# Kernel optimization log

Measured on AMD Instinct MI355X. Metric: run time of the kernel, lower is better.

The kernel has to match this reference:

```python
import jax, jax.numpy as jnp
import numpy as np

# --- config (mirrors the torch/keras module's config object) ---
RATIOS = np.array([0.5, 1.0, 2.0], dtype=np.float32)
SCALE = 128.0
POS_THRESH = 0.15
NMS_THRESH = 0.7
STRIDE = 16.0
H = W = 64
A = len(RATIOS)           # anchors per spatial location
N = H * W * A             # total anchors = 12288


def _conv(x, w, b):
    # NHWC input, HWIO kernel, SAME padding, stride 1
    y = jax.lax.conv_general_dilated(x, w, (1, 1), 'SAME',
                                     dimension_numbers=('NHWC', 'HWIO', 'NHWC'))
    return y + b


def _grid_anchors():
    ws = SCALE * np.sqrt(RATIOS)
    hs = SCALE / np.sqrt(RATIOS)
    base = np.stack([-ws / 2, -hs / 2, ws / 2, hs / 2], axis=1)      # [A,4]
    xs = (np.arange(W, dtype=np.float32) + 0.5) * STRIDE
    ys = (np.arange(H, dtype=np.float32) + 0.5) * STRIDE
    cx, cy = np.meshgrid(xs, ys)                                     # [H,W]
    shifts = np.stack([cx, cy, cx, cy], axis=-1).reshape(-1, 1, 4)   # [H*W,1,4]
    return jnp.asarray((shifts + base[None]).reshape(-1, 4).astype(np.float32))  # [N,4]


def _decode(anchors, deltas):
    # standard RPN box decode: (dx,dy,dw,dh) applied to (x1,y1,x2,y2) anchors
    w = anchors[:, 2] - anchors[:, 0]
    h = anchors[:, 3] - anchors[:, 1]
    xc = (anchors[:, 0] + anchors[:, 2]) * 0.5 + deltas[:, 0] * w
    yc = (anchors[:, 1] + anchors[:, 3]) * 0.5 + deltas[:, 1] * h
    nw = w * jnp.exp(deltas[:, 2])
    nh = h * jnp.exp(deltas[:, 3])
    return jnp.stack([xc - nw / 2, yc - nh / 2, xc + nw / 2, yc + nh / 2], axis=1)  # [N,4]


def _nms(boxes, keep0, thresh):
    # greedy NMS in index order (original passes scores=ones to tf NMS, so
    # the sort by score is a no-op and greedy order == index order).
    boxes = jax.lax.stop_gradient(boxes)
    x1, y1, x2, y2 = boxes[:, 0], boxes[:, 1], boxes[:, 2], boxes[:, 3]
    areas = (x2 - x1) * (y2 - y1)
    idx = jnp.arange(boxes.shape[0])

    def body(i, keep):
        xx1 = jnp.maximum(x1[i], x1)
        yy1 = jnp.maximum(y1[i], y1)
        xx2 = jnp.minimum(x2[i], x2)
        yy2 = jnp.minimum(y2[i], y2)
        inter = jnp.maximum(xx2 - xx1, 0.0) * jnp.maximum(yy2 - yy1, 0.0)
        iou = inter / (areas[i] + areas - inter + 1e-9)
        suppress = keep[i] & keep & (iou > thresh) & (idx > i)
        return keep & ~suppress

    return jax.lax.fori_loop(0, boxes.shape[0], body, keep0)


def setup_inputs() -> dict:
    key = jax.random.key(0)
    ks = jax.random.split(key, 7)
    c_in, c_mid = 1024, 512
    inputs = jax.random.normal(ks[0], (1, H, W, c_in), dtype=jnp.float32)
    conv_w = jax.random.normal(ks[1], (3, 3, c_in, c_mid), dtype=jnp.float32) * 0.01
    conv_b = jnp.zeros((c_mid,), dtype=jnp.float32)
    cls_w = jax.random.normal(ks[2], (1, 1, c_mid, 2 * A), dtype=jnp.float32) * 0.05
    cls_b = jnp.zeros((2 * A,), dtype=jnp.float32)
    reg_w = jax.random.normal(ks[3], (1, 1, c_mid, 4 * A), dtype=jnp.float32) * 0.01
    reg_b = jnp.zeros((4 * A,), dtype=jnp.float32)
    return {"inputs": inputs, "conv_w": conv_w, "conv_b": conv_b,
            "cls_w": cls_w, "cls_b": cls_b, "reg_w": reg_w, "reg_b": reg_b}


def reference(inputs, conv_w, conv_b, cls_w, cls_b, reg_w, reg_b):
    x = jax.nn.relu(_conv(inputs, conv_w, conv_b))                  # [1,H,W,512]
    cls = jax.nn.softmax(_conv(x, cls_w, cls_b), axis=-1)           # [1,H,W,2A]
    reg = _conv(x, reg_w, reg_b)                                    # [1,H,W,4A]
    scores = cls.reshape(-1, 2)[:, 1]                               # [N] fg prob
    deltas = reg.reshape(-1, 4)                                     # [N,4]
    boxes = _decode(_grid_anchors(), deltas)                        # [N,4]
    keep0 = scores > POS_THRESH
    keep = _nms(boxes, keep0, NMS_THRESH)                           # [N] bool
    # fixed-shape proposal output: suppressed / filtered boxes zeroed out
    return boxes * keep[:, None].astype(boxes.dtype)
```

## Files before the change

### kernel.cpp

```cpp
#include <hip/hip_runtime.h>
#include <cstdint>

#define NBOX 12288
#define NWORDS 192
#define POS_THRESH 0.15f
#define NMS_THRESH 0.7f

typedef unsigned long long u64;
typedef _Float16 half8 __attribute__((ext_vector_type(8)));
typedef float floatx4 __attribute__((ext_vector_type(4)));

__global__ __launch_bounds__(256) void zero_y(float4* __restrict__ Y) {
  Y[blockIdx.x * 256 + threadIdx.x] = float4{0.f, 0.f, 0.f, 0.f};
}

__global__ __launch_bounds__(256) void prep_wt(
    const float* __restrict__ Wc, _Float16* __restrict__ WTh, _Float16* __restrict__ WTl)
{
  __shared__ float tile[64][65];
  const int b = blockIdx.x;
  const int tap = b >> 7;
  const int rem = b & 127;
  const int c0 = (rem >> 3) * 64, n0 = (rem & 7) * 64;
  const int t = threadIdx.x;
  #pragma unroll
  for (int i = 0; i < 16; ++i) {
    const int idx = i * 256 + t;
    const int c = idx >> 6, n = idx & 63;
    tile[n][c] = Wc[((size_t)(tap * 1024 + c0 + c)) * 512 + n0 + n];
  }
  __syncthreads();
  #pragma unroll
  for (int i = 0; i < 16; ++i) {
    const int idx = i * 256 + t;
    const int n = idx >> 6, c = idx & 63;
    const float v = tile[n][c];
    const _Float16 h = (_Float16)v;
    const _Float16 l = (_Float16)((v - (float)h) * 4096.0f);
    const size_t o = ((size_t)(tap * 512 + n0 + n)) * 1024 + c0 + c;
    WTh[o] = h;
    WTl[o] = l;
  }
}

#define AROW 40
#define AS_PLANE (4 * 66 * AROW)
#define BS_PLANE (128 * AROW)
#define YPLANE 2097152
__global__ __launch_bounds__(256, 2) void conv_mfma(
    const float* __restrict__ X, const _Float16* __restrict__ WTh,
    const _Float16* __restrict__ WTl, float* __restrict__ Y, int partial)
{
  __shared__ _Float16 As[2 * AS_PLANE];
  __shared__ _Float16 Bs[2 * BS_PLANE];
  const int bid = blockIdx.x;
  const int ks = bid & 3;
  const int nt = (bid >> 2) & 3;
  const int mt = bid >> 4;
  const int t = threadIdx.x;
  const int lane = t & 63, wid = t >> 6;
  const int wm = wid >> 1, wn = wid & 1;
  const int lrow = lane & 15, quad = lane >> 4;

  floatx4 accH[4][4], accL[4][4];
  #pragma unroll
  for (int i = 0; i < 4; ++i)
    #pragma unroll
    for (int j = 0; j < 4; ++j) { accH[i][j] = (floatx4)0.f; accL[i][j] = (floatx4)0.f; }

  for (int kc = 0; kc < 8; ++kc) {
    const int c0 = ks * 256 + kc * 32;
    __syncthreads();
    for (int r = t; r < 264; r += 256) {
      const int yy = r / 66;
      const int xx = r - yy * 66;
      const int yi = mt * 2 + yy - 1;
      const int xi = xx - 1;
      const int akey = (r >> 3) & 3;
      _Float16* dsth = &As[r * AROW];
      _Float16* dstl = dsth + AS_PLANE;
      if (yi >= 0 && yi < 64 && xi >= 0 && xi < 64) {
        const float4* src = (const float4*)(X + ((size_t)(yi * 64 + xi)) * 1024 + c0);
        #pragma unroll
        for (int j = 0; j < 4; ++j) {
          const float4 va = src[2 * j], vb = src[2 * j + 1];
          const float f[8] = {va.x, va.y, va.z, va.w, vb.x, vb.y, vb.z, vb.w};
          half8 hh, hl;
          #pragma unroll
          for (int e = 0; e < 8; ++e) {
            const _Float16 h = (_Float16)f[e];
            hh[e] = h;
            hl[e] = (_Float16)((f[e] - (float)h) * 4096.0f);
          }
          const int sl = (j ^ akey) * 8;
          *(half8*)&dsth[sl] = hh;
          *(half8*)&dstl[sl] = hl;
        }
      } else {
        const half8 z = (half8)(_Float16)0.f;
        #pragma unroll
        for (int j = 0; j < 4; ++j) { *(half8*)&dsth[j * 8] = z; *(half8*)&dstl[j * 8] = z; }
      }
    }
    for (int tap = 0; tap < 9; ++tap) {
      if (tap > 0) __syncthreads();
      {
        const int hl = t >> 7, n = t & 127;
        const int bkey = (n >> 3) & 3;
        const _Float16* src = (hl ? WTl : WTh) +
            ((size_t)(tap * 512 + nt * 128 + n)) * 1024 + c0;
        _Float16* dst = &Bs[hl * BS_PLANE + n * AROW];
        #pragma unroll
        for (int j = 0; j < 4; ++j)
          *(half8*)&dst[(j ^ bkey) * 8] = *(const half8*)&src[j * 8];
      }
      __syncthreads();
      const int dy = tap / 3 - 1, dx = tap - (tap / 3) * 3 - 1;
      const int yy = wm + dy + 1;
      const int xxb = dx + 1;
      half8 Ah[4], Al[4], Bh[4], Bl[4];
      #pragma unroll
      for (int fm = 0; fm < 4; ++fm) {
        const int row = yy * 66 + xxb + fm * 16 + lrow;
        const int idx = row * AROW + ((quad ^ ((row >> 3) & 3)) * 8);
        Ah[fm] = *(const half8*)&As[idx];
        Al[fm] = *(const half8*)&As[idx + AS_PLANE];
      }
      #pragma unroll
      for (int fn = 0; fn < 4; ++fn) {
        const int row = wn * 64 + fn * 16 + lrow;
        const int idx = row * AROW + ((quad ^ ((row >> 3) & 3)) * 8);
        Bh[fn] = *(const half8*)&Bs[idx];
        Bl[fn] = *(const half8*)&Bs[idx + BS_PLANE];
      }
      #pragma unroll
      for (int fm = 0; fm < 4; ++fm)
        #pragma unroll
        for (int fn = 0; fn < 4; ++fn) {
          accH[fm][fn] = __builtin_amdgcn_mfma_f32_16x16x32_f16(Ah[fm], Bh[fn], accH[fm][fn], 0, 0, 0);
          accL[fm][fn] = __builtin_amdgcn_mfma_f32_16x16x32_f16(Al[fm], Bh[fn], accL[fm][fn], 0, 0, 0);
          accL[fm][fn] = __builtin_amdgcn_mfma_f32_16x16x32_f16(Ah[fm], Bl[fn], accL[fm][fn], 0, 0, 0);
        }
    }
  }
  const int m0 = mt * 128 + wm * 64;
  const int n0 = nt * 128 + wn * 64;
  if (partial) {
    float* Yp = Y + (size_t)ks * YPLANE;
    #pragma unroll
    for (int fm = 0; fm < 4; ++fm)
      #pragma unroll
      for (int fn = 0; fn < 4; ++fn) {
        const int n = n0 + fn * 16 + lrow;
        #pragma unroll
        for (int r = 0; r < 4; ++r) {
          const int m = m0 + fm * 16 + quad * 4 + r;
          Yp[(size_t)m * 512 + n] = accH[fm][fn][r] + accL[fm][fn][r] * (1.0f / 4096.0f);
        }
      }
  } else {
    #pragma unroll
    for (int fm = 0; fm < 4; ++fm)
      #pragma unroll
      for (int fn = 0; fn < 4; ++fn) {
        const int n = n0 + fn * 16 + lrow;
        #pragma unroll
        for (int r = 0; r < 4; ++r) {
          const int m = m0 + fm * 16 + quad * 4 + r;
          atomicAdd(&Y[(size_t)m * 512 + n],
                    accH[fm][fn][r] + accL[fm][fn][r] * (1.0f / 4096.0f));
        }
      }
  }
}

__global__ __launch_bounds__(64) void heads_decode(
    const float* __restrict__ Yx, int nparts, const float* __restrict__ Bc,
    const float* __restrict__ Wcls, const float* __restrict__ bcls,
    const float* __restrict__ Wreg, const float* __restrict__ breg,
    float* __restrict__ boxes, float* __restrict__ scores, int* __restrict__ ext)
{
  __shared__ float xs[512];
  const int pos = blockIdx.x;
  const int l = threadIdx.x;
  if (l == 0 && pos < NWORDS) ext[pos] = pos;
  float4 v0 = {0.f, 0.f, 0.f, 0.f};
  float4 v1 = {0.f, 0.f, 0.f, 0.f};
  for (int p = 0; p < nparts; ++p) {
    const float* xrow = Yx + (size_t)p * YPLANE + (size_t)pos * 512;
    const float4 a = *(const float4*)&xrow[l * 8];
    const float4 b = *(const float4*)&xrow[l * 8 + 4];
    v0.x += a.x; v0.y += a.y; v0.z += a.z; v0.w += a.w;
    v1.x += b.x; v1.y += b.y; v1.z += b.z; v1.w += b.w;
  }
  const float4 b0 = *(const float4*)&Bc[l * 8];
  const float4 b1 = *(const float4*)&Bc[l * 8 + 4];
  xs[l * 8 + 0] = fmaxf(v0.x + b0.x, 0.f);
  xs[l * 8 + 1] = fmaxf(v0.y + b0.y, 0.f);
  xs[l * 8 + 2] = fmaxf(v0.z + b0.z, 0.f);
  xs[l * 8 + 3] = fmaxf(v0.w + b0.w, 0.f);
  xs[l * 8 + 4] = fmaxf(v1.x + b1.x, 0.f);
  xs[l * 8 + 5] = fmaxf(v1.y + b1.y, 0.f);
  xs[l * 8 + 6] = fmaxf(v1.z + b1.z, 0.f);
  xs[l * 8 + 7] = fmaxf(v1.w + b1.w, 0.f);
  __syncthreads();

  const float* wp;
  int oc;
  float bini;
  if (l < 6)       { wp = Wcls + l;       oc = 6;  bini = bcls[l]; }
  else if (l < 18) { wp = Wreg + (l - 6); oc = 12; bini = breg[l - 6]; }
  else             { wp = Wcls;           oc = 0;  bini = 0.f; }
  float acc = bini;
  const float* p = wp;
  #pragma unroll 4
  for (int c = 0; c < 512; ++c) { acc = fmaf(xs[c], *p, acc); p += oc; }

  const float l0 = __shfl(acc, 0), l1 = __shfl(acc, 1), l2 = __shfl(acc, 2);
  const float l3 = __shfl(acc, 3), l4 = __shfl(acc, 4), l5 = __shfl(acc, 5);
  const int a = (l < 3) ? l : 0;
  const float d0 = __shfl(acc, 6 + a * 4 + 0);
  const float d1 = __shfl(acc, 6 + a * 4 + 1);
  const float d2 = __shfl(acc, 6 + a * 4 + 2);
  const float d3 = __shfl(acc, 6 + a * 4 + 3);

  const float mx = fmaxf(fmaxf(fmaxf(l0, l1), fmaxf(l2, l3)), fmaxf(l4, l5));
  const float e0 = expf(l0 - mx), e1 = expf(l1 - mx), e2 = expf(l2 - mx);
  const float e3 = expf(l3 - mx), e4 = expf(l4 - mx), e5 = expf(l5 - mx);
  const float den = ((((e0 + e1) + e2) + e3) + e4) + e5;
  const float esel = (a == 0) ? e1 : ((a == 1) ? e3 : e5);
  const float sc = esel / den;

  const int px = pos & 63, py = pos >> 6;
  const float cx = (px + 0.5f) * 16.0f;
  const float cy = (py + 0.5f) * 16.0f;
  const float ratio = (a == 0) ? 0.5f : ((a == 1) ? 1.0f : 2.0f);
  const float sq = sqrtf(ratio);
  const float wsz = 128.0f * sq;
  const float hsz = 128.0f / sq;
  const float a0 = cx - wsz * 0.5f;
  const float a1 = cy - hsz * 0.5f;
  const float a2 = cx + wsz * 0.5f;
  const float a3 = cy + hsz * 0.5f;
  const float w = a2 - a0, h = a3 - a1;
  const float xc = __fadd_rn(__fmul_rn(__fadd_rn(a0, a2), 0.5f), __fmul_rn(d0, w));
  const float yc = __fadd_rn(__fmul_rn(__fadd_rn(a1, a3), 0.5f), __fmul_rn(d1, h));
  const float nw = __fmul_rn(w, expf(d2));
  const float nh = __fmul_rn(h, expf(d3));
  float4 box;
  box.x = __fsub_rn(xc, __fmul_rn(nw, 0.5f));
  box.y = __fsub_rn(yc, __fmul_rn(nh, 0.5f));
  box.z = __fadd_rn(xc, __fmul_rn(nw, 0.5f));
  box.w = __fadd_rn(yc, __fmul_rn(nh, 0.5f));

  if (l < 3) {
    const int idx = pos * 3 + a;
    *(float4*)&boxes[idx * 4] = box;
    scores[idx] = sc;
  }
}

__global__ __launch_bounds__(256) void build_mask(
    const float* __restrict__ boxes, u64* __restrict__ maskT,
    int* __restrict__ ext)
{
  const int w  = blockIdx.x;
  const int ci = blockIdx.y;
  if (w < ci) return;
  __shared__ float4 rb[64];
  __shared__ int anyf;
  const int t = threadIdx.x;
  const int lane = t & 63, wid = t >> 6;
  if (t == 0) anyf = 0;
  if (t < 64) rb[t] = *(const float4*)&boxes[(ci * 64 + t) * 4];
  const float4 cb = *(const float4*)&boxes[(w * 64 + lane) * 4];
  const float careaa = __fmul_rn(cb.z - cb.x, cb.w - cb.y);
  const int jglob = w * 64 + lane;
  __syncthreads();
  bool any = false;
  for (int rr = 0; rr < 16; ++rr) {
    const int r = wid * 16 + rr;
    const int row = ci * 64 + r;
    const float4 rx = rb[r];
    const float ra = __fmul_rn(rx.z - rx.x, rx.w - rx.y);
    const float xx1 = fmaxf(rx.x, cb.x);
    const float yy1 = fmaxf(rx.y, cb.y);
    const float xx2 = fminf(rx.z, cb.z);
    const float yy2 = fminf(rx.w, cb.w);
    const float iw = fmaxf(__fsub_rn(xx2, xx1), 0.f);
    const float ih = fmaxf(__fsub_rn(yy2, yy1), 0.f);
    const float inter = __fmul_rn(iw, ih);
    const float den = __fadd_rn(__fsub_rn(__fadd_rn(ra, careaa), inter), 1e-9f);
    const float iou = __fdiv_rn(inter, den);
    const bool bit = (iou > NMS_THRESH) && (jglob > row);
    any |= bit;
    const u64 word = __ballot(bit ? 1 : 0);
    if (lane == 0) maskT[(size_t)w * NBOX + row] = word;
  }
  if (any) anyf = 1;
  __syncthreads();
  if (t == 0 && anyf && w > ci) atomicMax(&ext[ci], w);
}

__device__ __forceinline__ u64 rl64(unsigned lo, unsigned hi, int l) {
  const unsigned a = (unsigned)__builtin_amdgcn_readlane((int)lo, l);
  const unsigned b = (unsigned)__builtin_amdgcn_readlane((int)hi, l);
  return ((u64)b << 32) | (u64)a;
}

#define NSTEP(C_, MU, DU, MP, DP)                                               \
  do {                                                                          \
    const int c_ = (C_);                                                        \
    const int e_ = extS[c_];                                                    \
    const u64 aw0v_ = alive[c_];                                                \
           \
    if (c_ + 1 < NWORDS) {                                                      \
      DP = maskT[(size_t)(c_ + 1) * NBOX + (size_t)(c_ + 1) * 64 + lane];       \
      const int en_ = extS[c_ + 1];                                             \
      const int t0n_ = c_ + 2 + wsub;                                           \
      if (t0n_ <= en_) {                                                        \
        const u64* cbp_ = maskT + (size_t)t0n_ * NBOX + (size_t)(c_ + 1) * 64 + sub * 8; \
        MP##0 = cbp_[0]; MP##1 = cbp_[1]; MP##2 = cbp_[2]; MP##3 = cbp_[3];     \
        MP##4 = cbp_[4]; MP##5 = cbp_[5]; MP##6 = cbp_[6]; MP##7 = cbp_[7];     \
      }                                                                         \
    }                                                                           \
     \
    const unsigned awlo_ = (unsigned)__builtin_amdgcn_readfirstlane((int)(unsigned)(aw0v_ & 0xffffffffull)); \
    const unsigned awhi_ = (unsigned)__builtin_amdgcn_readfirstlane((int)(unsigned)(aw0v_ >> 32)); \
    const u64 aw0_ = ((u64)awhi_ << 32) | (u64)awlo_;                           \
    if (aw0_) {                                                                 \
      const unsigned dlo_ = (unsigned)(DU & 0xffffffffull);                     \
      const unsigned dhi_ = (unsigned)(DU >> 32);                               \
      u64 aw_ = aw0_;                                                           \
      const bool sb_ = ((aw0_ >> lane) & 1ull) && ((DU & aw0_) != 0ull);        \
      u64 pending_ = __ballot(sb_ ? 1 : 0);                                     \
      while (pending_) {                                                        \
        const u64 p0_ = pending_;                                               \
        const u64 p1_ = p0_ & (p0_ - 1);                                        \
        const u64 p2_ = p1_ & (p1_ - 1);                                        \
        const u64 p3_ = p2_ & (p2_ - 1);                                        \
        const int b0_ = __builtin_ctzll(p0_);                                   \
        const int b1_ = p1_ ? __builtin_ctzll(p1_) : 64;                        \
        const int b2_ = p2_ ? __builtin_ctzll(p2_) : 64;                        \
        const int b3_ = p3_ ? __builtin_ctzll(p3_) : 64;                        \
        const u64 r0_ = rl64(dlo_, dhi_, b0_);                                  \
        const u64 r1_ = rl64(dlo_, dhi_, b1_ & 63);                             \
        const u64 r2_ = rl64(dlo_, dhi_, b2_ & 63);                             \
        const u64 r3_ = rl64(dlo_, dhi_, b3_ & 63);                             \
        u64 supp_ = r0_;                                                        \
        u64 done_ = 1ull << b0_;                                                \
        const u64 k1_ = ((b1_ < 64) & !((supp_ >> (b1_ & 63)) & 1ull)) ? ~0ull : 0ull; \
        supp_ |= r1_ & k1_;  done_ |= (1ull << (b1_ & 63)) & k1_;               \
        const u64 k2_ = ((b2_ < 64) & !((supp_ >> (b2_ & 63)) & 1ull)) ? ~0ull : 0ull; \
        supp_ |= r2_ & k2_;  done_ |= (1ull << (b2_ & 63)) & k2_;               \
        const u64 k3_ = ((b3_ < 64) & !((supp_ >> (b3_ & 63)) & 1ull)) ? ~0ull : 0ull; \
        supp_ |= r3_ & k3_;  done_ |= (1ull << (b3_ & 63)) & k3_;               \
        aw_ &= ~supp_;                                                          \
        pending_ &= ~(supp_ | done_);                                           \
      }                                                                         \
       \
      const int t0_ = c_ + 1 + wsub;                                            \
      if (t0_ <= e_) {                                                          \
        const unsigned oct_ = (unsigned)(aw_ >> (sub * 8)) & 0xffu;             \
        u64 sup_ = 0ull;                                                        \
        if (oct_ & 1u)   sup_ |= MU##0;                                         \
        if (oct_ & 2u)   sup_ |= MU##1;                                         \
        if (oct_ & 4u)   sup_ |= MU##2;                                         \
        if (oct_ & 8u)   sup_ |= MU##3;                                         \
        if (oct_ & 16u)  sup_ |= MU##4;                                         \
        if (oct_ & 32u)  sup_ |= MU##5;                                         \
        if (oct_ & 64u)  sup_ |= MU##6;                                         \
        if (oct_ & 128u) sup_ |= MU##7;                                         \
        if (sup_) atomicAnd((unsigned long long*)&alive[t0_], ~sup_);           \
      }                                                                         \
             \
      for (int base_ = c_ + 33; base_ <= e_; base_ += 32) {                     \
        const int tw_ = base_ + wsub;                                           \
        if (tw_ <= e_) {                                                        \
          const u64* cbp_ = maskT + (size_t)tw_ * NBOX + (size_t)c_ * 64 + sub * 8; \
          u64 m_[8];                                                            \
          _Pragma("unroll")                                                     \
          for (int j_ = 0; j_ < 8; ++j_) m_[j_] = cbp_[j_];                     \
          const unsigned oct_ = (unsigned)(aw_ >> (sub * 8)) & 0xffu;           \
          u64 sup_ = 0ull;                                                      \
          _Pragma("unroll")                                                     \
          for (int j_ = 0; j_ < 8; ++j_) if ((oct_ >> j_) & 1u) sup_ |= m_[j_]; \
          if (sup_) atomicAnd((unsigned long long*)&alive[tw_], ~sup_);         \
        }                                                                       \
      }                                                                         \
      if (t == 0) alive[c_] = aw_;                                              \
    }                                                                           \
         \
    asm volatile("s_waitcnt lgkmcnt(0)" ::: "memory");                          \
    __builtin_amdgcn_s_barrier();                                               \
    asm volatile("" ::: "memory");                                              \
  } while (0)

__global__ __launch_bounds__(256) void nms_scan(
    const float* __restrict__ scores, const u64* __restrict__ maskT,
    const int* __restrict__ ext, u64* __restrict__ aliveOut)
{
  __shared__ u64 alive[NWORDS];
  __shared__ int extS[NWORDS];
  const int t = threadIdx.x;
  const int lane = t & 63;
  const int wsub = t >> 3;
  const int sub = t & 7;
  if (t < NWORDS) {
    u64 wbits = 0ull;
    const float4* sp = (const float4*)(scores + t * 64);
    #pragma unroll
    for (int q = 0; q < 16; ++q) {
      const float4 s = sp[q];
      if (s.x > POS_THRESH) wbits |= (1ull << (q * 4 + 0));
      if (s.y > POS_THRESH) wbits |= (1ull << (q * 4 + 1));
      if (s.z > POS_THRESH) wbits |= (1ull << (q * 4 + 2));
      if (s.w > POS_THRESH) wbits |= (1ull << (q * 4 + 3));
    }
    alive[t] = wbits;
    extS[t] = ext[t];
  }
  u64 mA0 = 0, mA1 = 0, mA2 = 0, mA3 = 0, mA4 = 0, mA5 = 0, mA6 = 0, mA7 = 0;
  u64 mB0 = 0, mB1 = 0, mB2 = 0, mB3 = 0, mB4 = 0, mB5 = 0, mB6 = 0, mB7 = 0;
  u64 dgA = 0, dgB = 0;
  const int e0 = ext[0];
  if (1 + wsub <= e0) {
    const u64* cbp = maskT + (size_t)(1 + wsub) * NBOX + sub * 8;
    mA0 = cbp[0]; mA1 = cbp[1]; mA2 = cbp[2]; mA3 = cbp[3];
    mA4 = cbp[4]; mA5 = cbp[5]; mA6 = cbp[6]; mA7 = cbp[7];
  }
  dgA = maskT[lane];
  asm volatile("s_waitcnt lgkmcnt(0)" ::: "memory");
  __builtin_amdgcn_s_barrier();
  asm volatile("" ::: "memory");

  for (int c = 0; c < NWORDS; c += 2) {
    NSTEP(c,     mA, dgA, mB, dgB);
    NSTEP(c + 1, mB, dgB, mA, dgA);
  }
  if (t < NWORDS) aliveOut[t] = alive[t];
}

__global__ __launch_bounds__(256) void write_output(
    const float* __restrict__ boxes, const u64* __restrict__ alive,
    float* __restrict__ out)
{
  const int i = blockIdx.x * 256 + threadIdx.x;
  if (i < NBOX) {
    const bool k = (alive[i >> 6] >> (i & 63)) & 1ull;
    const float4 b = *(const float4*)&boxes[i * 4];
    const float4 z = {0.f, 0.f, 0.f, 0.f};
    *(float4*)&out[i * 4] = k ? b : z;
  }
}

extern "C" void kernel_launch(void* const* d_in, const int* in_sizes, int n_in,
                              void* d_out, int out_size, void* d_ws, size_t ws_size,
                              hipStream_t stream) {
  const float* X    = (const float*)d_in[0];
  const float* Wc   = (const float*)d_in[1];
  const float* Bc   = (const float*)d_in[2];
  const float* Wcls = (const float*)d_in[3];
  const float* bcls = (const float*)d_in[4];
  const float* Wreg = (const float*)d_in[5];
  const float* breg = (const float*)d_in[6];

  char* ws = (char*)d_ws;
  const size_t NEED_BIG = 52676864ull;

  if (ws_size >= NEED_BIG) {
    float*     Y4     = (float*)    (ws);
    float*     boxes  = (float*)    (ws + 33554432);
    float*     scores = (float*)    (ws + 33751040);
    u64*       aliveG = (u64*)      (ws + 33800192);
    int*       extG   = (int*)      (ws + 33801728);
    _Float16*  WTh    = (_Float16*) (ws + 33802496);
    _Float16*  WTl    = (_Float16*) (ws + 43239680);
    u64*       maskT  = (u64*)      (ws + 33802496);

    prep_wt     <<<1152, 256, 0, stream>>>(Wc, WTh, WTl);
    conv_mfma   <<<512, 256, 0, stream>>>(X, WTh, WTl, Y4, 1);
    heads_decode<<<4096, 64, 0, stream>>>(Y4, 4, Bc, Wcls, bcls, Wreg, breg, boxes, scores, extG);
    build_mask  <<<dim3(192, 192), 256, 0, stream>>>(boxes, maskT, extG);
    nms_scan    <<<1, 256, 0, stream>>>(scores, maskT, extG, aliveG);
    write_output<<<48, 256, 0, stream>>>(boxes, aliveG, (float*)d_out);
  } else {
    float*     Y      = (float*)    (ws);
    float*     boxes  = (float*)    (ws + 8388608);
    float*     scores = (float*)    (ws + 8585216);
    u64*       aliveG = (u64*)      (ws + 8634368);
    int*       extG   = (int*)      (ws + 8635904);
    _Float16*  WTh    = (_Float16*) (ws + 8636672);
    _Float16*  WTl    = (_Float16*) (ws + 18073856);
    u64*       maskT  = (u64*)      (ws + 8636672);

    zero_y      <<<2048, 256, 0, stream>>>((float4*)Y);
    prep_wt     <<<1152, 256, 0, stream>>>(Wc, WTh, WTl);
    conv_mfma   <<<512, 256, 0, stream>>>(X, WTh, WTl, Y, 0);
    heads_decode<<<4096, 64, 0, stream>>>(Y, 1, Bc, Wcls, bcls, Wreg, breg, boxes, scores, extG);
    build_mask  <<<dim3(192, 192), 256, 0, stream>>>(boxes, maskT, extG);
    nms_scan    <<<1, 256, 0, stream>>>(scores, maskT, extG, aliveG);
    write_output<<<48, 256, 0, stream>>>(boxes, aliveG, (float*)d_out);
  }
}
```

Before: 501.7 us.

## Replace serial NMS scan with parallel fixed-point iteration and sequential fallback

Result: faster. 490.5 us (-2.2%).

```diff
diff --git a/kernel.cpp b/kernel.cpp
--- a/kernel.cpp
+++ b/kernel.cpp
@@ -307,138 +307,253 @@
   const unsigned b = (unsigned)__builtin_amdgcn_readlane((int)hi, l);
   return ((u64)b << 32) | (u64)a;
 }
-
-#define NSTEP(C_, MU, DU, MP, DP)                                               \
+__device__ __forceinline__ u64 rl64v(u64 v, int ln) {
+  const unsigned a = (unsigned)__builtin_amdgcn_readlane((int)(unsigned)v, ln);
+  const unsigned b = (unsigned)__builtin_amdgcn_readlane((int)(unsigned)(v >> 32), ln);
+  return ((u64)b << 32) | (u64)a;
+}
+__device__ __forceinline__ u64 shflxor64(u64 v, int m) {
+  const int lo = __shfl_xor((int)(unsigned)v, m);
+  const int hi = __shfl_xor((int)(unsigned)(v >> 32), m);
+  return ((u64)(unsigned)hi << 32) | (unsigned)lo;
+}
+__device__ __forceinline__ u64 build_alive(const float* sp) {
+  u64 w = 0ull;
+  const float4* p = (const float4*)sp;
+  #pragma unroll
+  for (int q = 0; q < 16; ++q) {
+    const float4 s = p[q];
+    if (s.x > POS_THRESH) w |= (1ull << (q * 4 + 0));
+    if (s.y > POS_THRESH) w |= (1ull << (q * 4 + 1));
+    if (s.z > POS_THRESH) w |= (1ull << (q * 4 + 2));
+    if (s.w > POS_THRESH) w |= (1ull << (q * 4 + 3));
+  }
+  return w;
+}
+
+#define NSTEPF(C_, MU, DU, MP, DP)                                              \
   do {                                                                          \
-    const int c_ = (C_);                                                        \
-    const int e_ = extS[c_];                                                    \
-    const u64 aw0v_ = alive[c_];                                                \
-           \
-    if (c_ + 1 < NWORDS) {                                                      \
-      DP = maskT[(size_t)(c_ + 1) * NBOX + (size_t)(c_ + 1) * 64 + lane];       \
-      const int en_ = extS[c_ + 1];                                             \
-      const int t0n_ = c_ + 2 + wsub;                                           \
-      if (t0n_ <= en_) {                                                        \
-        const u64* cbp_ = maskT + (size_t)t0n_ * NBOX + (size_t)(c_ + 1) * 64 + sub * 8; \
-        MP##0 = cbp_[0]; MP##1 = cbp_[1]; MP##2 = cbp_[2]; MP##3 = cbp_[3];     \
-        MP##4 = cbp_[4]; MP##5 = cbp_[5]; MP##6 = cbp_[6]; MP##7 = cbp_[7];     \
+    if (t < 256) {                                                              \
+      const int c_ = (C_);                                                      \
+      const int e_ = extS[c_];                                                  \
+      const u64 aw0v_ = alvS[c_];                                               \
+      if (c_ + 1 < NWORDS) {                                                    \
+        DP = maskT[(size_t)(c_ + 1) * NBOX + (size_t)(c_ + 1) * 64 + lane];     \
+        const int en_ = extS[c_ + 1];                                           \
+        const int t0n_ = c_ + 2 + wsub;                                         \
+        if (t0n_ <= en_) {                                                      \
+          const u64* cbp_ = maskT + (size_t)t0n_ * NBOX + (size_t)(c_ + 1) * 64 + sub * 8; \
+          MP##0 = cbp_[0]; MP##1 = cbp_[1]; MP##2 = cbp_[2]; MP##3 = cbp_[3];   \
+          MP##4 = cbp_[4]; MP##5 = cbp_[5]; MP##6 = cbp_[6]; MP##7 = cbp_[7];   \
+        }                                                                       \
+      }                                                                         \
+      const unsigned awlo_ = (unsigned)__builtin_amdgcn_readfirstlane((int)(unsigned)(aw0v_ & 0xffffffffull)); \
+      const unsigned awhi_ = (unsigned)__builtin_amdgcn_readfirstlane((int)(unsigned)(aw0v_ >> 32)); \
+      const u64 aw0_ = ((u64)awhi_ << 32) | (u64)awlo_;                         \
+      if (aw0_) {                                                               \
+        const unsigned dlo_ = (unsigned)(DU & 0xffffffffull);                   \
+        const unsigned dhi_ = (unsigned)(DU >> 32);                             \
+        u64 aw_ = aw0_;                                                         \
+        const bool sb_ = ((aw0_ >> lane) & 1ull) && ((DU & aw0_) != 0ull);      \
+        u64 pending_ = __ballot(sb_ ? 1 : 0);                                   \
+        while (pending_) {                                                      \
+          const u64 p0_ = pending_;                                             \
+          const u64 p1_ = p0_ & (p0_ - 1);                                      \
+          const u64 p2_ = p1_ & (p1_ - 1);                                      \
+          const u64 p3_ = p2_ & (p2_ - 1);                                      \
+          const int b0_ = __builtin_ctzll(p0_);                                 \
+          const int b1_ = p1_ ? __builtin_ctzll(p1_) : 64;                      \
+          const int b2_ = p2_ ? __builtin_ctzll(p2_) : 64;                      \
+          const int b3_ = p3_ ? __builtin_ctzll(p3_) : 64;                      \
+          const u64 r0_ = rl64(dlo_, dhi_, b0_);                                \
+          const u64 r1_ = rl64(dlo_, dhi_, b1_ & 63);                           \
+          const u64 r2_ = rl64(dlo_, dhi_, b2_ & 63);                           \
+          const u64 r3_ = rl64(dlo_, dhi_, b3_ & 63);                           \
+          u64 supp_ = r0_;                                                      \
+          u64 done_ = 1ull << b0_;                                              \
+          const u64 k1_ = ((b1_ < 64) & !((supp_ >> (b1_ & 63)) & 1ull)) ? ~0ull : 0ull; \
+          supp_ |= r1_ & k1_;  done_ |= (1ull << (b1_ & 63)) & k1_;             \
+          const u64 k2_ = ((b2_ < 64) & !((supp_ >> (b2_ & 63)) & 1ull)) ? ~0ull : 0ull; \
+          supp_ |= r2_ & k2_;  done_ |= (1ull << (b2_ & 63)) & k2_;             \
+          const u64 k3_ = ((b3_ < 64) & !((supp_ >> (b3_ & 63)) & 1ull)) ? ~0ull : 0ull; \
+          supp_ |= r3_ & k3_;  done_ |= (1ull << (b3_ & 63)) & k3_;             \
+          aw_ &= ~supp_;                                                        \
+          pending_ &= ~(supp_ | done_);                                         \
+        }                                                                       \
+        const int t0_ = c_ + 1 + wsub;                                          \
+        if (t0_ <= e_) {                                                        \
+          const unsigned oct_ = (unsigned)(aw_ >> (sub * 8)) & 0xffu;           \
+          u64 sup_ = 0ull;                                                      \
+          if (oct_ & 1u)   sup_ |= MU##0;                                       \
+          if (oct_ & 2u)   sup_ |= MU##1;                                       \
+          if (oct_ & 4u)   sup_ |= MU##2;                                       \
+          if (oct_ & 8u)   sup_ |= MU##3;                                       \
+          if (oct_ & 16u)  sup_ |= MU##4;                                       \
+          if (oct_ & 32u)  sup_ |= MU##5;                                       \
+          if (oct_ & 64u)  sup_ |= MU##6;                                       \
+          if (oct_ & 128u) sup_ |= MU##7;                                       \
+          if (sup_) atomicAnd((unsigned long long*)&alvS[t0_], ~sup_);          \
+        }                                                                       \
+        for (int base_ = c_ + 33; base_ <= e_; base_ += 32) {                   \
+          const int tw_ = base_ + wsub;                                         \
+          if (tw_ <= e_) {                                                      \
+            const u64* cbp_ = maskT + (size_t)tw_ * NBOX + (size_t)c_ * 64 + sub * 8; \
+            u64 m_[8];                                                          \
+            _Pragma("unroll")                                                   \
+            for (int j_ = 0; j_ < 8; ++j_) m_[j_] = cbp_[j_];                   \
+            const unsigned oct_ = (unsigned)(aw_ >> (sub * 8)) & 0xffu;         \
+            u64 sup_ = 0ull;                                                    \
+            _Pragma("unroll")                                                   \
+            for (int j_ = 0; j_ < 8; ++j_) if ((oct_ >> j_) & 1u) sup_ |= m_[j_]; \
+            if (sup_) atomicAnd((unsigned long long*)&alvS[tw_], ~sup_);        \
+          }                                                                     \
+        }                                                                       \
+        if (t == 0) alvS[c_] = aw_;                                             \
       }                                                                         \
     }                                                                           \
-     \
-    const unsigned awlo_ = (unsigned)__builtin_amdgcn_readfirstlane((int)(unsigned)(aw0v_ & 0xffffffffull)); \
-    const unsigned awhi_ = (unsigned)__builtin_amdgcn_readfirstlane((int)(unsigned)(aw0v_ >> 32)); \
-    const u64 aw0_ = ((u64)awhi_ << 32) | (u64)awlo_;                           \
-    if (aw0_) {                                                                 \
-      const unsigned dlo_ = (unsigned)(DU & 0xffffffffull);                     \
-      const unsigned dhi_ = (unsigned)(DU >> 32);                               \
-      u64 aw_ = aw0_;                                                           \
-      const bool sb_ = ((aw0_ >> lane) & 1ull) && ((DU & aw0_) != 0ull);        \
-      u64 pending_ = __ballot(sb_ ? 1 : 0);                                     \
-      while (pending_) {                                                        \
-        const u64 p0_ = pending_;                                               \
-        const u64 p1_ = p0_ & (p0_ - 1);                                        \
-        const u64 p2_ = p1_ & (p1_ - 1);                                        \
-        const u64 p3_ = p2_ & (p2_ - 1);                                        \
-        const int b0_ = __builtin_ctzll(p0_);                                   \
-        const int b1_ = p1_ ? __builtin_ctzll(p1_) : 64;                        \
-        const int b2_ = p2_ ? __builtin_ctzll(p2_) : 64;                        \
-        const int b3_ = p3_ ? __builtin_ctzll(p3_) : 64;                        \
-        const u64 r0_ = rl64(dlo_, dhi_, b0_);                                  \
-        const u64 r1_ = rl64(dlo_, dhi_, b1_ & 63);                             \
-        const u64 r2_ = rl64(dlo_, dhi_, b2_ & 63);                             \
-        const u64 r3_ = rl64(dlo_, dhi_, b3_ & 63);                             \
-        u64 supp_ = r0_;                                                        \
-        u64 done_ = 1ull << b0_;                                                \
-        const u64 k1_ = ((b1_ < 64) & !((supp_ >> (b1_ & 63)) & 1ull)) ? ~0ull : 0ull; \
-        supp_ |= r1_ & k1_;  done_ |= (1ull << (b1_ & 63)) & k1_;               \
-        const u64 k2_ = ((b2_ < 64) & !((supp_ >> (b2_ & 63)) & 1ull)) ? ~0ull : 0ull; \
-        supp_ |= r2_ & k2_;  done_ |= (1ull << (b2_ & 63)) & k2_;               \
-        const u64 k3_ = ((b3_ < 64) & !((supp_ >> (b3_ & 63)) & 1ull)) ? ~0ull : 0ull; \
-        supp_ |= r3_ & k3_;  done_ |= (1ull << (b3_ & 63)) & k3_;               \
-        aw_ &= ~supp_;                                                          \
-        pending_ &= ~(supp_ | done_);                                           \
-      }                                                                         \
-       \
-      const int t0_ = c_ + 1 + wsub;                                            \
-      if (t0_ <= e_) {                                                          \
-        const unsigned oct_ = (unsigned)(aw_ >> (sub * 8)) & 0xffu;             \
-        u64 sup_ = 0ull;                                                        \
-        if (oct_ & 1u)   sup_ |= MU##0;                                         \
-        if (oct_ & 2u)   sup_ |= MU##1;                                         \
-        if (oct_ & 4u)   sup_ |= MU##2;                                         \
-        if (oct_ & 8u)   sup_ |= MU##3;                                         \
-        if (oct_ & 16u)  sup_ |= MU##4;                                         \
-        if (oct_ & 32u)  sup_ |= MU##5;                                         \
-        if (oct_ & 64u)  sup_ |= MU##6;                                         \
-        if (oct_ & 128u) sup_ |= MU##7;                                         \
-        if (sup_) atomicAnd((unsigned long long*)&alive[t0_], ~sup_);           \
-      }                                                                         \
-             \
-      for (int base_ = c_ + 33; base_ <= e_; base_ += 32) {                     \
-        const int tw_ = base_ + wsub;                                           \
-        if (tw_ <= e_) {                                                        \
-          const u64* cbp_ = maskT + (size_t)tw_ * NBOX + (size_t)c_ * 64 + sub * 8; \
-          u64 m_[8];                                                            \
-          _Pragma("unroll")                                                     \
-          for (int j_ = 0; j_ < 8; ++j_) m_[j_] = cbp_[j_];                     \
-          const unsigned oct_ = (unsigned)(aw_ >> (sub * 8)) & 0xffu;           \
-          u64 sup_ = 0ull;                                                      \
-          _Pragma("unroll")                                                     \
-          for (int j_ = 0; j_ < 8; ++j_) if ((oct_ >> j_) & 1u) sup_ |= m_[j_]; \
-          if (sup_) atomicAnd((unsigned long long*)&alive[tw_], ~sup_);         \
-        }                                                                       \
-      }                                                                         \
-      if (t == 0) alive[c_] = aw_;                                              \
-    }                                                                           \
-         \
     asm volatile("s_waitcnt lgkmcnt(0)" ::: "memory");                          \
     __builtin_amdgcn_s_barrier();                                               \
     asm volatile("" ::: "memory");                                              \
   } while (0)
 
-__global__ __launch_bounds__(256) void nms_scan(
+__global__ __launch_bounds__(1024) void nms_scan(
     const float* __restrict__ scores, const u64* __restrict__ maskT,
     const int* __restrict__ ext, u64* __restrict__ aliveOut)
 {
-  __shared__ u64 alive[NWORDS];
-  __shared__ int extS[NWORDS];
+  __shared__ u64 alvA[NWORDS], alvB[NWORDS], keep0S[NWORDS];
+  __shared__ int extS[NWORDS], srcLoS[NWORDS];
+  __shared__ int changedS;
   const int t = threadIdx.x;
   const int lane = t & 63;
+  const int wv = t >> 6;
+  const int g = lane >> 3;
+  const int s = lane & 7;
   const int wsub = t >> 3;
   const int sub = t & 7;
+
   if (t < NWORDS) {
-    u64 wbits = 0ull;
-    const float4* sp = (const float4*)(scores + t * 64);
-    #pragma unroll
-    for (int q = 0; q < 16; ++q) {
-      const float4 s = sp[q];
-      if (s.x > POS_THRESH) wbits |= (1ull << (q * 4 + 0));
-      if (s.y > POS_THRESH) wbits |= (1ull << (q * 4 + 1));
-      if (s.z > POS_THRESH) wbits |= (1ull << (q * 4 + 2));
-      if (s.w > POS_THRESH) wbits |= (1ull << (q * 4 + 3));
+    const u64 wb = build_alive(scores + (size_t)t * 64);
+    keep0S[t] = wb;
+    alvA[t] = wb;
+    extS[t] = ext[t];
+  }
+  if (t == 0) changedS = 0;
+  __syncthreads();
+  if (t < NWORDS) {
+    int lo = t;
+    for (int c = 0; c < t; ++c) if (extS[c] >= t) { lo = c; break; }
+    srcLoS[t] = lo;
+  }
+  __syncthreads();
+
+  int cur = 0, converged = 0;
+  for (int it = 0; it < 64; ++it) {
+    const u64* aOld = cur ? alvB : alvA;
+    u64* aNew = cur ? alvA : alvB;
+    for (int k = 0; k < 12; ++k) {
+      const int w = wv + k * 16;
+      const u64 dg = maskT[(size_t)w * NBOX + (size_t)w * 64 + lane];
+      const int lo = srcLoS[w];
+      u64 supx = 0ull;
+      for (int base = lo; base < w; base += 8) {
+        const int c = base + g;
+        u64 part = 0ull;
+        if (c < w) {
+          const u64 av = aOld[c];
+          const unsigned oct = (unsigned)((av >> (s * 8)) & 0xffull);
+          const u64* col = maskT + (size_t)w * NBOX + (size_t)c * 64 + s * 8;
+          const u64 m0 = col[0], m1 = col[1], m2 = col[2], m3 = col[3];
+          const u64 m4 = col[4], m5 = col[5], m6 = col[6], m7 = col[7];
+          if (oct & 1u)   part |= m0;
+          if (oct & 2u)   part |= m1;
+          if (oct & 4u)   part |= m2;
+          if (oct & 8u)   part |= m3;
+          if (oct & 16u)  part |= m4;
+          if (oct & 32u)  part |= m5;
+          if (oct & 64u)  part |= m6;
+          if (oct & 128u) part |= m7;
+        }
+        part |= shflxor64(part, 1);
+        part |= shflxor64(part, 2);
+        part |= shflxor64(part, 4);
+        part |= shflxor64(part, 8);
+        part |= shflxor64(part, 16);
+        part |= shflxor64(part, 32);
+        supx |= part;
+      }
+      const u64 b0v = keep0S[w] & ~supx;
+      u64 aw = b0v;
+      const bool sbv = ((b0v >> lane) & 1ull) && ((dg & b0v) != 0ull);
+      u64 pending = __ballot(sbv ? 1 : 0);
+      while (pending) {
+        const u64 q0 = pending;
+        const u64 q1 = q0 & (q0 - 1);
+        const u64 q2 = q1 & (q1 - 1);
+        const u64 q3 = q2 & (q2 - 1);
+        const int c0 = __builtin_ctzll(q0);
+        const int c1 = q1 ? __builtin_ctzll(q1) : 64;
+        const int c2 = q2 ? __builtin_ctzll(q2) : 64;
+        const int c3 = q3 ? __builtin_ctzll(q3) : 64;
+        const u64 u0 = rl64v(dg, c0);
+        const u64 u1 = rl64v(dg, c1 & 63);
+        const u64 u2 = rl64v(dg, c2 & 63);
+        const u64 u3 = rl64v(dg, c3 & 63);
+        u64 sp = u0;
+        u64 dn = 1ull << c0;
+        const u64 g1 = ((c1 < 64) && !((sp >> (c1 & 63)) & 1ull)) ? ~0ull : 0ull;
+        sp |= u1 & g1; dn |= (1ull << (c1 & 63)) & g1;
+        const u64 g2 = ((c2 < 64) && !((sp >> (c2 & 63)) & 1ull)) ? ~0ull : 0ull;
+        sp |= u2 & g2; dn |= (1ull << (c2 & 63)) & g2;
+        const u64 g3 = ((c3 < 64) && !((sp >> (c3 & 63)) & 1ull)) ? ~0ull : 0ull;
+        sp |= u3 & g3; dn |= (1ull << (c3 & 63)) & g3;
+        aw &= ~sp;
+        pending &= ~(sp | dn);
+      }
+      if (lane == 0) {
+        aNew[w] = aw;
+        if (aw != aOld[w]) changedS = 1;
+      }
     }
-    alive[t] = wbits;
-    extS[t] = ext[t];
-  }
+    __syncthreads();
+    const int ch = changedS;
+    __syncthreads();
+    cur ^= 1;
+    if (!ch) { converged = 1; break; }
+    if (t == 0) changedS = 0;
+    __syncthreads();
+  }
+
+  if (converged) {
+    const u64* fin = cur ? alvB : alvA;
+    if (t < NWORDS) aliveOut[t] = fin[t];
+    return;
+  }
+
+  u64* alvS = alvA;
+  if (t < NWORDS) alvS[t] = keep0S[t];
+  __syncthreads();
+
   u64 mA0 = 0, mA1 = 0, mA2 = 0, mA3 = 0, mA4 = 0, mA5 = 0, mA6 = 0, mA7 = 0;
   u64 mB0 = 0, mB1 = 0, mB2 = 0, mB3 = 0, mB4 = 0, mB5 = 0, mB6 = 0, mB7 = 0;
   u64 dgA = 0, dgB = 0;
-  const int e0 = ext[0];
-  if (1 + wsub <= e0) {
-    const u64* cbp = maskT + (size_t)(1 + wsub) * NBOX + sub * 8;
-    mA0 = cbp[0]; mA1 = cbp[1]; mA2 = cbp[2]; mA3 = cbp[3];
-    mA4 = cbp[4]; mA5 = cbp[5]; mA6 = cbp[6]; mA7 = cbp[7];
-  }
-  dgA = maskT[lane];
+  if (t < 256) {
+    const int e0f = extS[0];
+    if (1 + wsub <= e0f) {
+      const u64* cbp = maskT + (size_t)(1 + wsub) * NBOX + sub * 8;
+      mA0 = cbp[0]; mA1 = cbp[1]; mA2 = cbp[2]; mA3 = cbp[3];
+      mA4 = cbp[4]; mA5 = cbp[5]; mA6 = cbp[6]; mA7 = cbp[7];
+    }
+    dgA = maskT[lane];
+  }
   asm volatile("s_waitcnt lgkmcnt(0)" ::: "memory");
   __builtin_amdgcn_s_barrier();
   asm volatile("" ::: "memory");
 
   for (int c = 0; c < NWORDS; c += 2) {
-    NSTEP(c,     mA, dgA, mB, dgB);
-    NSTEP(c + 1, mB, dgB, mA, dgA);
-  }
-  if (t < NWORDS) aliveOut[t] = alive[t];
+    NSTEPF(c,     mA, dgA, mB, dgB);
+    NSTEPF(c + 1, mB, dgB, mA, dgA);
+  }
+  if (t < NWORDS) aliveOut[t] = alvS[t];
 }
 
 __global__ __launch_bounds__(256) void write_output(
@@ -482,7 +597,7 @@
     conv_mfma   <<<512, 256, 0, stream>>>(X, WTh, WTl, Y4, 1);
     heads_decode<<<4096, 64, 0, stream>>>(Y4, 4, Bc, Wcls, bcls, Wreg, breg, boxes, scores, extG);
     build_mask  <<<dim3(192, 192), 256, 0, stream>>>(boxes, maskT, extG);
-    nms_scan    <<<1, 256, 0, stream>>>(scores, maskT, extG, aliveG);
+    nms_scan    <<<1, 1024, 0, stream>>>(scores, maskT, extG, aliveG);
     write_output<<<48, 256, 0, stream>>>(boxes, aliveG, (float*)d_out);
   } else {
     float*     Y      = (float*)    (ws);
@@ -499,7 +614,7 @@
     conv_mfma   <<<512, 256, 0, stream>>>(X, WTh, WTl, Y, 0);
     heads_decode<<<4096, 64, 0, stream>>>(Y, 1, Bc, Wcls, bcls, Wreg, breg, boxes, scores, extG);
     build_mask  <<<dim3(192, 192), 256, 0, stream>>>(boxes, maskT, extG);
-    nms_scan    <<<1, 256, 0, stream>>>(scores, maskT, extG, aliveG);
+    nms_scan    <<<1, 1024, 0, stream>>>(scores, maskT, extG, aliveG);
     write_output<<<48, 256, 0, stream>>>(boxes, aliveG, (float*)d_out);
   }
 }
```
